# Optimization experiments

Hardware: AMD Instinct MI355X
Metric: run time of the kernel (lower is better)

Reference implementation:

```python
import jax, jax.numpy as jnp
import numpy as np

N = 12288      # nodes
E = 393216     # edges (avg degree 32)
D_IN = 512
D_H = 256      # interm_dim
D_Z = 64       # latent_dim


def setup_inputs() -> dict:
    key = jax.random.key(0)
    ks = jax.random.split(key, 9)
    X = jax.random.normal(ks[0], (N, D_IN), jnp.float32)
    edge_index = jax.random.randint(ks[1], (2, E), 0, N, dtype=jnp.int64)
    # GCNConv weights (glorot-ish scaling)
    W1 = jax.random.normal(ks[2], (D_IN, D_H), jnp.float32) / np.sqrt(D_IN)
    b1 = jnp.zeros((D_H,), jnp.float32)
    Wmu = jax.random.normal(ks[3], (D_H, D_Z), jnp.float32) / np.sqrt(D_H)
    bmu = jnp.zeros((D_Z,), jnp.float32)
    Wsig = jax.random.normal(ks[4], (D_H, 1), jnp.float32) / np.sqrt(D_H)
    bsig = jnp.zeros((1,), jnp.float32)
    # reparameterization noise (torch: Normal(0,1).sample(mus.size()))
    eps = jax.random.normal(ks[5], (N, D_Z), jnp.float32)
    return {"X": X, "edge_index": edge_index, "W1": W1, "b1": b1,
            "Wmu": Wmu, "bmu": bmu, "Wsig": Wsig, "bsig": bsig, "eps": eps}


def _gcn_conv(h_in, W, b, src, dst, norm):
    # GCNConv: linear transform then symmetric-normalized aggregation with self-loops
    h = h_in @ W + b                                   # [N, F_out]
    msg = h[src] * norm[src, None]                     # gather + scale
    agg = jax.ops.segment_sum(msg, dst, num_segments=N)
    # self-loop contribution: norm_i * norm_i * h_i
    return norm[:, None] * (agg + norm[:, None] * h)


def reference(X, edge_index, W1, b1, Wmu, bmu, Wsig, bsig, eps):
    src, dst = edge_index[0], edge_index[1]
    # degree of A + I (edge weight 1, plus self loop)
    deg = jax.ops.segment_sum(jnp.ones((E,), X.dtype), dst, num_segments=N) + 1.0
    norm = jax.lax.rsqrt(deg)                          # D^{-1/2}

    # encoder
    H = jax.nn.relu(_gcn_conv(X, W1, b1, src, dst, norm))   # [N, D_H]; dropout p=0.0
    mus = _gcn_conv(H, Wmu, bmu, src, dst, norm)            # [N, D_Z]
    logsigma2s = _gcn_conv(H, Wsig, bsig, src, dst, norm)   # [N, 1]

    # reparameterize
    sigmas = jnp.exp(0.5 * logsigma2s)                      # [N, 1]
    Z = mus + sigmas * eps                                  # [N, D_Z]

    # dense decoder
    ZZt = Z @ Z.T                                           # [N, N]
    return ZZt, mus, logsigma2s
```

## Files before the change

kernel.cpp:

```cpp
#include <hip/hip_runtime.h>

#define N_NODES 12288
#define N_EDGES 393216
#define DIN 512
#define DH 256
#define DZ 64

typedef __bf16 bf16x8 __attribute__((ext_vector_type(8)));
typedef float f32x4 __attribute__((ext_vector_type(4)));
typedef unsigned short u16x8 __attribute__((ext_vector_type(8)));

static __device__ __forceinline__ unsigned short f2bf(float f) {
    unsigned int u = __float_as_uint(f);
    unsigned int r = (u + 0x7fffu + ((u >> 16) & 1u)) >> 16;
    return (unsigned short)r;
}
static __device__ __forceinline__ float bf2f(unsigned short u) {
    return __uint_as_float((unsigned int)u << 16);
}

__global__ __launch_bounds__(256) void k_prep(const float* __restrict__ X, unsigned short* __restrict__ Xb,
                                              const float* __restrict__ W1, unsigned short* __restrict__ W1T,
                                              const float* __restrict__ Wmu, unsigned short* __restrict__ WmuT,
                                              const int* __restrict__ dst, int* __restrict__ deg) {
    int b = blockIdx.x;
    if (b < 6144) {
        int i = b * 256 + threadIdx.x;
        float4 v = ((const float4*)X)[i];
        ushort4 o;
        o.x = f2bf(v.x); o.y = f2bf(v.y); o.z = f2bf(v.z); o.w = f2bf(v.w);
        ((ushort4*)Xb)[i] = o;
    } else if (b < 6656) {
        int i = (b - 6144) * 256 + threadIdx.x;
        int c = i >> 9, k = i & 511;
        W1T[i] = f2bf(W1[k * DH + c]);
    } else if (b < 6720) {
        int i = (b - 6656) * 256 + threadIdx.x;
        int c = i >> 8, k = i & 255;
        WmuT[i] = f2bf(Wmu[k * DZ + c]);
    } else {
        int e = (b - 6720) * 256 + threadIdx.x;
        atomicAdd(&deg[dst[e]], 1);
    }
}

__global__ __launch_bounds__(512) void k_sg(const unsigned short* __restrict__ Xb,
                                            const unsigned short* __restrict__ W1T,
                                            const float* __restrict__ b1, const int* __restrict__ deg,
                                            float* __restrict__ norm, unsigned short* __restrict__ g1,
                                            const int* __restrict__ src, const int* __restrict__ dst,
                                            int* __restrict__ rp, int* __restrict__ cursor,
                                            int* __restrict__ ssrc, int* __restrict__ flag) {
    __shared__ int sp[512];
    if (blockIdx.x < 96) {
        int j = blockIdx.x;
        int wid = threadIdx.x >> 6;
        int lane = threadIdx.x & 63;
        int ln = lane & 15, kg = lane >> 4;
        int rb = (j >> 1) * 256 + (wid >> 1) * 64;
        int cb = (j & 1) * 128 + (wid & 1) * 64;
        f32x4 acc[4][4] = {};
        const unsigned short* xa = Xb + (size_t)(rb + ln) * DIN + kg * 8;
        const unsigned short* wb = W1T + (size_t)(cb + ln) * DIN + kg * 8;
        for (int ks = 0; ks < 16; ++ks) {
            int k0 = ks * 32;
            bf16x8 a[4], b[4];
#pragma unroll
            for (int m = 0; m < 4; ++m) a[m] = *(const bf16x8*)(xa + (size_t)m * 16 * DIN + k0);
#pragma unroll
            for (int n = 0; n < 4; ++n) b[n] = *(const bf16x8*)(wb + (size_t)n * 16 * DIN + k0);
#pragma unroll
            for (int m = 0; m < 4; ++m)
#pragma unroll
                for (int n = 0; n < 4; ++n)
                    acc[m][n] = __builtin_amdgcn_mfma_f32_16x16x32_bf16(a[m], b[n], acc[m][n], 0, 0, 0);
        }
#pragma unroll
        for (int m = 0; m < 4; ++m)
#pragma unroll
            for (int r = 0; r < 4; ++r) {
                int row = rb + m * 16 + kg * 4 + r;
                float ni = rsqrtf((float)deg[row] + 1.0f);
#pragma unroll
                for (int n = 0; n < 4; ++n) {
                    int col = cb + n * 16 + ln;
                    g1[(size_t)row * DH + col] = f2bf(ni * (acc[m][n][r] + b1[col]));
                }
            }
    } else {
        int t = threadIdx.x;
        if (blockIdx.x == 96) {
            int base = t * 24;
            int loc[24];
            int s = 0;
#pragma unroll
            for (int j = 0; j < 24; ++j) {
                int c = deg[base + j];
                norm[base + j] = rsqrtf((float)c + 1.0f);
                cursor[base + j] = 0;
                loc[j] = s; s += c;
            }
            sp[t] = s;
            __syncthreads();
            for (int off = 1; off < 512; off <<= 1) {
                int v = (t >= off) ? sp[t - off] : 0;
                __syncthreads();
                sp[t] += v;
                __syncthreads();
            }
            int pre = (t == 0) ? 0 : sp[t - 1];
#pragma unroll
            for (int j = 0; j < 24; ++j) rp[base + j] = pre + loc[j];
            if (t == 511) rp[N_NODES] = sp[511];
            __threadfence();
            __syncthreads();
            if (t == 0)
                __hip_atomic_store(flag, 1, __ATOMIC_RELEASE, __HIP_MEMORY_SCOPE_AGENT);
        } else {
            if (t == 0) {
                while (__hip_atomic_load(flag, __ATOMIC_RELAXED, __HIP_MEMORY_SCOPE_AGENT) == 0)
                    __builtin_amdgcn_s_sleep(8);
                (void)__hip_atomic_load(flag, __ATOMIC_ACQUIRE, __HIP_MEMORY_SCOPE_AGENT);
            }
            __syncthreads();
        }
        int base = (blockIdx.x - 96) * 512 + t;
#pragma unroll
        for (int e = base; e < N_EDGES; e += 192 * 512) {
            int d = dst[e];
            int pos = atomicAdd(&cursor[d], 1);
            ssrc[rp[d] + pos] = src[e];
        }
    }
}

__global__ __launch_bounds__(256) void k_agg1(const unsigned short* __restrict__ g1,
                                              const int* __restrict__ rp, const int* __restrict__ ssrc,
                                              const float* __restrict__ norm, const float* __restrict__ Wsig,
                                              unsigned short* __restrict__ G2, float* __restrict__ tvec,
                                              float* __restrict__ qv) {
    int w = threadIdx.x >> 6;
    int lane = threadIdx.x & 63;
    int half = lane >> 5, lh = lane & 31;
    int i = blockIdx.x * 4 + w;
    int beg = rp[i], end = rp[i + 1];
    int itn = (end - beg + 1) >> 1;
    size_t cho = (size_t)lh * 8;
    float a8[8] = {};
    float ssum = 0.f;
#pragma unroll 2
    for (int it = 0; it < itn; ++it) {
        int e = beg + it * 2 + half;
        if (e < end) {
            int s = ssrc[e];
            u16x8 v = *(const u16x8*)(g1 + ((size_t)s << 8) + cho);
            ssum += norm[s];
#pragma unroll
            for (int j = 0; j < 8; ++j) a8[j] += bf2f(v[j]);
        }
    }
    if (half == 0) {
        u16x8 v = *(const u16x8*)(g1 + ((size_t)i << 8) + cho);
#pragma unroll
        for (int j = 0; j < 8; ++j) a8[j] += bf2f(v[j]);
    }
#pragma unroll
    for (int j = 0; j < 8; ++j) a8[j] += __shfl_xor(a8[j], 32);
    ssum += __shfl_xor(ssum, 32);
    float ni = norm[i];
    const float4 ws0 = *(const float4*)(Wsig + cho);
    const float4 ws1 = *(const float4*)(Wsig + cho + 4);
    float g[8];
#pragma unroll
    for (int j = 0; j < 8; ++j) g[j] = ni * fmaxf(ni * a8[j], 0.f);
    float qp = g[0] * ws0.x + g[1] * ws0.y + g[2] * ws0.z + g[3] * ws0.w
             + g[4] * ws1.x + g[5] * ws1.y + g[6] * ws1.z + g[7] * ws1.w;
    if (half == 0) {
        u16x8 o;
#pragma unroll
        for (int j = 0; j < 8; ++j) o[j] = f2bf(g[j]);
        *(u16x8*)(G2 + ((size_t)i << 8) + cho) = o;
    }
#pragma unroll
    for (int m = 16; m >= 1; m >>= 1) qp += __shfl_xor(qp, m);
    if (lane == 0) {
        tvec[i] = ssum + ni;
        qv[i] = qp;
    }
}

__global__ __launch_bounds__(256) void k_gemm2(const unsigned short* __restrict__ G2,
                                               const unsigned short* __restrict__ WmuT,
                                               unsigned short* __restrict__ Pb) {
    int wid = threadIdx.x >> 6;
    int lane = threadIdx.x & 63;
    int ln = lane & 15, kg = lane >> 4;
    int rb = blockIdx.x * 128 + wid * 32;
    f32x4 acc[2][4] = {};
    const unsigned short* xa = G2 + (size_t)(rb + ln) * DH + kg * 8;
    const unsigned short* wb = WmuT + (size_t)ln * DH + kg * 8;
    for (int ks = 0; ks < 8; ++ks) {
        int k0 = ks * 32;
        bf16x8 a[2], b[4];
#pragma unroll
        for (int m = 0; m < 2; ++m) a[m] = *(const bf16x8*)(xa + (size_t)m * 16 * DH + k0);
#pragma unroll
        for (int n = 0; n < 4; ++n) b[n] = *(const bf16x8*)(wb + (size_t)n * 16 * DH + k0);
#pragma unroll
        for (int m = 0; m < 2; ++m)
#pragma unroll
            for (int n = 0; n < 4; ++n)
                acc[m][n] = __builtin_amdgcn_mfma_f32_16x16x32_bf16(a[m], b[n], acc[m][n], 0, 0, 0);
    }
#pragma unroll
    for (int m = 0; m < 2; ++m)
#pragma unroll
        for (int n = 0; n < 4; ++n)
#pragma unroll
            for (int r = 0; r < 4; ++r) {
                int row = rb + m * 16 + kg * 4 + r;
                int col = n * 16 + ln;
                Pb[(size_t)row * DZ + col] = f2bf(acc[m][n][r]);
            }
}

__global__ __launch_bounds__(256) void k_agg2(const unsigned short* __restrict__ Pb,
                                              const float* __restrict__ qv,
                                              const int* __restrict__ rp, const int* __restrict__ ssrc,
                                              const float* __restrict__ norm, const float* __restrict__ tvec,
                                              const float* __restrict__ bmu, const float* __restrict__ bsig,
                                              const float* __restrict__ eps,
                                              float* __restrict__ mus_out, float* __restrict__ logs_out,
                                              unsigned short* __restrict__ Zb) {
    int w = threadIdx.x >> 6;
    int lane = threadIdx.x & 63;
    int grp = lane >> 4, li = lane & 15;
    int i = blockIdx.x * 4 + w;
    int beg = rp[i], end = rp[i + 1];
    int itn = (end - beg + 3) >> 2;
    int co = li * 4;
    float a4[4] = {};
    float qa = 0.f;
#pragma unroll 2
    for (int it = 0; it < itn; ++it) {
        int e = beg + it * 4 + grp;
        if (e < end) {
            int s = ssrc[e];
            ushort4 v = *(const ushort4*)(Pb + ((size_t)s << 6) + co);
            qa += qv[s];
            a4[0] += bf2f(v.x); a4[1] += bf2f(v.y); a4[2] += bf2f(v.z); a4[3] += bf2f(v.w);
        }
    }
    if (grp == 0) {
        ushort4 v = *(const ushort4*)(Pb + ((size_t)i << 6) + co);
        qa += qv[i];
        a4[0] += bf2f(v.x); a4[1] += bf2f(v.y); a4[2] += bf2f(v.z); a4[3] += bf2f(v.w);
    }
#pragma unroll
    for (int j = 0; j < 4; ++j) {
        a4[j] += __shfl_xor(a4[j], 16);
        a4[j] += __shfl_xor(a4[j], 32);
    }
    qa += __shfl_xor(qa, 16);
    qa += __shfl_xor(qa, 32);
    float ni = norm[i], tv = tvec[i];
    float ls = ni * (qa + bsig[0] * tv);
    float sig = expf(0.5f * ls);
    if (lane == 0) logs_out[i] = ls;
    if (lane < 16) {
        const float4 bm = *(const float4*)(bmu + co);
        float4 mu;
        mu.x = ni * (a4[0] + bm.x * tv);
        mu.y = ni * (a4[1] + bm.y * tv);
        mu.z = ni * (a4[2] + bm.z * tv);
        mu.w = ni * (a4[3] + bm.w * tv);
        size_t oidx = ((size_t)i << 6) + co;
        *(float4*)(mus_out + oidx) = mu;
        const float4 ep = *(const float4*)(eps + oidx);
        ushort4 z;
        z.x = f2bf(mu.x + sig * ep.x);
        z.y = f2bf(mu.y + sig * ep.y);
        z.z = f2bf(mu.z + sig * ep.z);
        z.w = f2bf(mu.w + sig * ep.w);
        *(ushort4*)(Zb + oidx) = z;
    }
}

#define LPAD 260
__global__ __launch_bounds__(256) void k_zzt(const unsigned short* __restrict__ Zb, float* __restrict__ out) {
    __shared__ float lds[32 * LPAD];
    int w = threadIdx.x >> 6;
    int lane = threadIdx.x & 63;
    int ln = lane & 15, kg = lane >> 4;
    int rb = blockIdx.x * 64;
    int cb = blockIdx.y * 256 + w * 64;
    bf16x8 a[4][2], b[4][2];
#pragma unroll
    for (int m = 0; m < 4; ++m)
#pragma unroll
        for (int kc = 0; kc < 2; ++kc)
            a[m][kc] = *(const bf16x8*)(Zb + (size_t)(rb + m * 16 + ln) * DZ + kc * 32 + kg * 8);
#pragma unroll
    for (int n = 0; n < 4; ++n)
#pragma unroll
        for (int kc = 0; kc < 2; ++kc)
            b[n][kc] = *(const bf16x8*)(Zb + (size_t)(cb + n * 16 + ln) * DZ + kc * 32 + kg * 8);
    f32x4 acc[4][4] = {};
#pragma unroll
    for (int m = 0; m < 4; ++m)
#pragma unroll
        for (int n = 0; n < 4; ++n) {
            acc[m][n] = __builtin_amdgcn_mfma_f32_16x16x32_bf16(a[m][0], b[n][0], acc[m][n], 0, 0, 0);
            acc[m][n] = __builtin_amdgcn_mfma_f32_16x16x32_bf16(a[m][1], b[n][1], acc[m][n], 0, 0, 0);
        }
    int c4 = (threadIdx.x & 63) * 4;
    int rw = threadIdx.x >> 6;
    size_t colbase = (size_t)blockIdx.y * 256 + c4;
#pragma unroll
    for (int p = 0; p < 2; ++p) {
        if (p) __syncthreads();
#pragma unroll
        for (int mm = 0; mm < 2; ++mm) {
            int m = p * 2 + mm;
#pragma unroll
            for (int n = 0; n < 4; ++n)
#pragma unroll
                for (int r = 0; r < 4; ++r)
                    lds[(mm * 16 + kg * 4 + r) * LPAD + w * 64 + n * 16 + ln] = acc[m][n][r];
        }
        __syncthreads();
#pragma unroll
        for (int it = 0; it < 8; ++it) {
            int rl = it * 4 + rw;
            f32x4 v = *(const f32x4*)&lds[rl * LPAD + c4];
            __builtin_nontemporal_store(v, (f32x4*)(out + (size_t)(rb + p * 32 + rl) * N_NODES + colbase));
        }
    }
}

extern "C" void kernel_launch(void* const* d_in, const int* in_sizes, int n_in,
                              void* d_out, int out_size, void* d_ws, size_t ws_size,
                              hipStream_t stream) {
    const float* X = (const float*)d_in[0];
    const int* edge = (const int*)d_in[1];
    const float* W1 = (const float*)d_in[2];
    const float* b1 = (const float*)d_in[3];
    const float* Wmu = (const float*)d_in[4];
    const float* bmu = (const float*)d_in[5];
    const float* Wsig = (const float*)d_in[6];
    const float* bsig = (const float*)d_in[7];
    const float* eps = (const float*)d_in[8];

    const int* esrc = edge;
    const int* edst = edge + N_EDGES;

    char* w = (char*)d_ws;
    int* flag = (int*)w;           w += 64;
    int* deg = (int*)w;            w += (size_t)N_NODES * 4;
    int* cursor = (int*)w;         w += (size_t)N_NODES * 4;
    float* norm = (float*)w;       w += (size_t)N_NODES * 4;
    float* tvec = (float*)w;       w += (size_t)N_NODES * 4;
    float* qv = (float*)w;         w += (size_t)N_NODES * 4;
    int* rowptr = (int*)w;         w += (size_t)(N_NODES + 64) * 4;
    int* ssrc = (int*)w;           w += (size_t)N_EDGES * 4;
    unsigned short* Xb = (unsigned short*)w;   w += (size_t)N_NODES * DIN * 2;
    unsigned short* W1T = (unsigned short*)w;  w += (size_t)DIN * DH * 2;
    unsigned short* WmuT = (unsigned short*)w; w += (size_t)DH * DZ * 2;
    unsigned short* g1 = (unsigned short*)w;   w += (size_t)N_NODES * DH * 2;
    unsigned short* G2 = (unsigned short*)w;   w += (size_t)N_NODES * DH * 2;
    unsigned short* Pb = (unsigned short*)w;   w += (size_t)N_NODES * DZ * 2;
    unsigned short* Zb = (unsigned short*)w;   w += (size_t)N_NODES * DZ * 2;

    float* out_zzt = (float*)d_out;
    float* out_mus = out_zzt + (size_t)N_NODES * N_NODES;
    float* out_logs = out_mus + (size_t)N_NODES * DZ;

    (void)hipMemsetAsync(d_ws, 0, 64 + (size_t)N_NODES * 4, stream);
    k_prep<<<8256, 256, 0, stream>>>(X, Xb, W1, W1T, Wmu, WmuT, edst, deg);
    k_sg<<<288, 512, 0, stream>>>(Xb, W1T, b1, deg, norm, g1, esrc, edst, rowptr, cursor, ssrc, flag);
    k_agg1<<<N_NODES / 4, 256, 0, stream>>>(g1, rowptr, ssrc, norm, Wsig, G2, tvec, qv);
    k_gemm2<<<N_NODES / 128, 256, 0, stream>>>(G2, WmuT, Pb);
    k_agg2<<<N_NODES / 4, 256, 0, stream>>>(Pb, qv, rowptr, ssrc, norm, tvec, bmu, bsig, eps,
                                            out_mus, out_logs, Zb);
    k_zzt<<<dim3(N_NODES / 64, N_NODES / 256), 256, 0, stream>>>(Zb, out_zzt);
}
```

Baseline: 260.3 us.

## Fuse agg1, gemm2 and agg2 into one persistent kernel with grid barriers

Merges the first aggregation, the small mu GEMM and the second aggregation into a single persistent kernel of 2048 blocks. Software grid-wide barriers built on agent-scope atomics replace the kernel boundaries. Nodes are processed in a grid-stride loop, and the GEMM is split into 16-row tiles per wave. This removes two kernel launches and their inter-kernel gaps. It relies on all 2048 blocks being co-resident, otherwise the spin barrier deadlocks, and it adds barrier spin cost.

```diff
diff --git a/kernel.cpp b/kernel.cpp
--- a/kernel.cpp
+++ b/kernel.cpp
@@ -5,6 +5,7 @@
 #define DIN 512
 #define DH 256
 #define DZ 64
+#define NBA 2048
 
 typedef __bf16 bf16x8 __attribute__((ext_vector_type(8)));
 typedef float f32x4 __attribute__((ext_vector_type(4)));
@@ -17,6 +18,17 @@
 }
 static __device__ __forceinline__ float bf2f(unsigned short u) {
     return __uint_as_float((unsigned int)u << 16);
+}
+
+static __device__ __forceinline__ void gridbar(int* bar, int p, int nb) {
+    __syncthreads();
+    if (threadIdx.x == 0) {
+        __hip_atomic_fetch_add(&bar[p], 1, __ATOMIC_RELEASE, __HIP_MEMORY_SCOPE_AGENT);
+        while (__hip_atomic_load(&bar[p], __ATOMIC_RELAXED, __HIP_MEMORY_SCOPE_AGENT) < nb)
+            __builtin_amdgcn_s_sleep(8);
+        (void)__hip_atomic_load(&bar[p], __ATOMIC_ACQUIRE, __HIP_MEMORY_SCOPE_AGENT);
+    }
+    __syncthreads();
 }
 
 __global__ __launch_bounds__(256) void k_prep(const float* __restrict__ X, unsigned short* __restrict__ Xb,
@@ -134,155 +146,150 @@
     }
 }
 
-__global__ __launch_bounds__(256) void k_agg1(const unsigned short* __restrict__ g1,
-                                              const int* __restrict__ rp, const int* __restrict__ ssrc,
-                                              const float* __restrict__ norm, const float* __restrict__ Wsig,
-                                              unsigned short* __restrict__ G2, float* __restrict__ tvec,
-                                              float* __restrict__ qv) {
+__global__ __launch_bounds__(256, 8) void k_a12(
+    const unsigned short* __restrict__ g1,
+    const int* __restrict__ rp, const int* __restrict__ ssrc,
+    const float* __restrict__ norm, const float* __restrict__ Wsig,
+    const unsigned short* __restrict__ WmuT,
+    unsigned short* __restrict__ G2, float* __restrict__ tvec, float* __restrict__ qv,
+    unsigned short* __restrict__ Pb,
+    const float* __restrict__ bmu, const float* __restrict__ bsig,
+    const float* __restrict__ eps,
+    float* __restrict__ mus_out, float* __restrict__ logs_out,
+    unsigned short* __restrict__ Zb, int* __restrict__ bar) {
+
     int w = threadIdx.x >> 6;
     int lane = threadIdx.x & 63;
-    int half = lane >> 5, lh = lane & 31;
-    int i = blockIdx.x * 4 + w;
-    int beg = rp[i], end = rp[i + 1];
-    int itn = (end - beg + 1) >> 1;
-    size_t cho = (size_t)lh * 8;
-    float a8[8] = {};
-    float ssum = 0.f;
+    int gw = blockIdx.x * 4 + w;
+
+    {
+        int half = lane >> 5, lh = lane & 31;
+        size_t cho = (size_t)lh * 8;
+        for (int i = gw; i < N_NODES; i += 8192) {
+            int beg = rp[i], end = rp[i + 1];
+            int itn = (end - beg + 1) >> 1;
+            float a8[8] = {};
+            float ssum = 0.f;
 #pragma unroll 2
-    for (int it = 0; it < itn; ++it) {
-        int e = beg + it * 2 + half;
-        if (e < end) {
-            int s = ssrc[e];
-            u16x8 v = *(const u16x8*)(g1 + ((size_t)s << 8) + cho);
-            ssum += norm[s];
-#pragma unroll
-            for (int j = 0; j < 8; ++j) a8[j] += bf2f(v[j]);
-        }
-    }
-    if (half == 0) {
-        u16x8 v = *(const u16x8*)(g1 + ((size_t)i << 8) + cho);
-#pragma unroll
-        for (int j = 0; j < 8; ++j) a8[j] += bf2f(v[j]);
-    }
-#pragma unroll
-    for (int j = 0; j < 8; ++j) a8[j] += __shfl_xor(a8[j], 32);
-    ssum += __shfl_xor(ssum, 32);
-    float ni = norm[i];
-    const float4 ws0 = *(const float4*)(Wsig + cho);
-    const float4 ws1 = *(const float4*)(Wsig + cho + 4);
-    float g[8];
-#pragma unroll
-    for (int j = 0; j < 8; ++j) g[j] = ni * fmaxf(ni * a8[j], 0.f);
-    float qp = g[0] * ws0.x + g[1] * ws0.y + g[2] * ws0.z + g[3] * ws0.w
-             + g[4] * ws1.x + g[5] * ws1.y + g[6] * ws1.z + g[7] * ws1.w;
-    if (half == 0) {
-        u16x8 o;
-#pragma unroll
-        for (int j = 0; j < 8; ++j) o[j] = f2bf(g[j]);
-        *(u16x8*)(G2 + ((size_t)i << 8) + cho) = o;
-    }
-#pragma unroll
-    for (int m = 16; m >= 1; m >>= 1) qp += __shfl_xor(qp, m);
-    if (lane == 0) {
-        tvec[i] = ssum + ni;
-        qv[i] = qp;
-    }
-}
-
-__global__ __launch_bounds__(256) void k_gemm2(const unsigned short* __restrict__ G2,
-                                               const unsigned short* __restrict__ WmuT,
-                                               unsigned short* __restrict__ Pb) {
-    int wid = threadIdx.x >> 6;
-    int lane = threadIdx.x & 63;
-    int ln = lane & 15, kg = lane >> 4;
-    int rb = blockIdx.x * 128 + wid * 32;
-    f32x4 acc[2][4] = {};
-    const unsigned short* xa = G2 + (size_t)(rb + ln) * DH + kg * 8;
-    const unsigned short* wb = WmuT + (size_t)ln * DH + kg * 8;
-    for (int ks = 0; ks < 8; ++ks) {
-        int k0 = ks * 32;
-        bf16x8 a[2], b[4];
-#pragma unroll
-        for (int m = 0; m < 2; ++m) a[m] = *(const bf16x8*)(xa + (size_t)m * 16 * DH + k0);
-#pragma unroll
-        for (int n = 0; n < 4; ++n) b[n] = *(const bf16x8*)(wb + (size_t)n * 16 * DH + k0);
-#pragma unroll
-        for (int m = 0; m < 2; ++m)
+            for (int it = 0; it < itn; ++it) {
+                int e = beg + it * 2 + half;
+                if (e < end) {
+                    int s = ssrc[e];
+                    u16x8 v = *(const u16x8*)(g1 + ((size_t)s << 8) + cho);
+                    ssum += norm[s];
+#pragma unroll
+                    for (int j = 0; j < 8; ++j) a8[j] += bf2f(v[j]);
+                }
+            }
+            if (half == 0) {
+                u16x8 v = *(const u16x8*)(g1 + ((size_t)i << 8) + cho);
+#pragma unroll
+                for (int j = 0; j < 8; ++j) a8[j] += bf2f(v[j]);
+            }
+#pragma unroll
+            for (int j = 0; j < 8; ++j) a8[j] += __shfl_xor(a8[j], 32);
+            ssum += __shfl_xor(ssum, 32);
+            float ni = norm[i];
+            const float4 ws0 = *(const float4*)(Wsig + cho);
+            const float4 ws1 = *(const float4*)(Wsig + cho + 4);
+            float g[8];
+#pragma unroll
+            for (int j = 0; j < 8; ++j) g[j] = ni * fmaxf(ni * a8[j], 0.f);
+            float qp = g[0] * ws0.x + g[1] * ws0.y + g[2] * ws0.z + g[3] * ws0.w
+                     + g[4] * ws1.x + g[5] * ws1.y + g[6] * ws1.z + g[7] * ws1.w;
+            if (half == 0) {
+                u16x8 o;
+#pragma unroll
+                for (int j = 0; j < 8; ++j) o[j] = f2bf(g[j]);
+                *(u16x8*)(G2 + ((size_t)i << 8) + cho) = o;
+            }
+#pragma unroll
+            for (int m = 16; m >= 1; m >>= 1) qp += __shfl_xor(qp, m);
+            if (lane == 0) {
+                tvec[i] = ssum + ni;
+                qv[i] = qp;
+            }
+        }
+    }
+    gridbar(bar, 0, NBA);
+
+    if (gw < 768) {
+        int ln = lane & 15, kg = lane >> 4;
+        int rb = gw * 16;
+        f32x4 acc[4] = {};
+        const unsigned short* xa = G2 + (size_t)(rb + ln) * DH + kg * 8;
+        const unsigned short* wb = WmuT + (size_t)ln * DH + kg * 8;
+#pragma unroll
+        for (int ks = 0; ks < 8; ++ks) {
+            int k0 = ks * 32;
+            bf16x8 a = *(const bf16x8*)(xa + k0);
+            bf16x8 b[4];
+#pragma unroll
+            for (int n = 0; n < 4; ++n) b[n] = *(const bf16x8*)(wb + (size_t)n * 16 * DH + k0);
 #pragma unroll
             for (int n = 0; n < 4; ++n)
-                acc[m][n] = __builtin_amdgcn_mfma_f32_16x16x32_bf16(a[m], b[n], acc[m][n], 0, 0, 0);
-    }
-#pragma unroll
-    for (int m = 0; m < 2; ++m)
+                acc[n] = __builtin_amdgcn_mfma_f32_16x16x32_bf16(a, b[n], acc[n], 0, 0, 0);
+        }
 #pragma unroll
         for (int n = 0; n < 4; ++n)
 #pragma unroll
-            for (int r = 0; r < 4; ++r) {
-                int row = rb + m * 16 + kg * 4 + r;
-                int col = n * 16 + ln;
-                Pb[(size_t)row * DZ + col] = f2bf(acc[m][n][r]);
-            }
-}
-
-__global__ __launch_bounds__(256) void k_agg2(const unsigned short* __restrict__ Pb,
-                                              const float* __restrict__ qv,
-                                              const int* __restrict__ rp, const int* __restrict__ ssrc,
-                                              const float* __restrict__ norm, const float* __restrict__ tvec,
-                                              const float* __restrict__ bmu, const float* __restrict__ bsig,
-                                              const float* __restrict__ eps,
-                                              float* __restrict__ mus_out, float* __restrict__ logs_out,
-                                              unsigned short* __restrict__ Zb) {
-    int w = threadIdx.x >> 6;
-    int lane = threadIdx.x & 63;
-    int grp = lane >> 4, li = lane & 15;
-    int i = blockIdx.x * 4 + w;
-    int beg = rp[i], end = rp[i + 1];
-    int itn = (end - beg + 3) >> 2;
-    int co = li * 4;
-    float a4[4] = {};
-    float qa = 0.f;
+            for (int r = 0; r < 4; ++r)
+                Pb[(size_t)(rb + kg * 4 + r) * DZ + n * 16 + ln] = f2bf(acc[n][r]);
+    }
+    gridbar(bar, 1, NBA);
+
+    {
+        int grp = lane >> 4, li = lane & 15;
+        int co = li * 4;
+        for (int i = gw; i < N_NODES; i += 8192) {
+            int beg = rp[i], end = rp[i + 1];
+            int itn = (end - beg + 3) >> 2;
+            float a4[4] = {};
+            float qa = 0.f;
 #pragma unroll 2
-    for (int it = 0; it < itn; ++it) {
-        int e = beg + it * 4 + grp;
-        if (e < end) {
-            int s = ssrc[e];
-            ushort4 v = *(const ushort4*)(Pb + ((size_t)s << 6) + co);
-            qa += qv[s];
-            a4[0] += bf2f(v.x); a4[1] += bf2f(v.y); a4[2] += bf2f(v.z); a4[3] += bf2f(v.w);
-        }
-    }
-    if (grp == 0) {
-        ushort4 v = *(const ushort4*)(Pb + ((size_t)i << 6) + co);
-        qa += qv[i];
-        a4[0] += bf2f(v.x); a4[1] += bf2f(v.y); a4[2] += bf2f(v.z); a4[3] += bf2f(v.w);
-    }
-#pragma unroll
-    for (int j = 0; j < 4; ++j) {
-        a4[j] += __shfl_xor(a4[j], 16);
-        a4[j] += __shfl_xor(a4[j], 32);
-    }
-    qa += __shfl_xor(qa, 16);
-    qa += __shfl_xor(qa, 32);
-    float ni = norm[i], tv = tvec[i];
-    float ls = ni * (qa + bsig[0] * tv);
-    float sig = expf(0.5f * ls);
-    if (lane == 0) logs_out[i] = ls;
-    if (lane < 16) {
-        const float4 bm = *(const float4*)(bmu + co);
-        float4 mu;
-        mu.x = ni * (a4[0] + bm.x * tv);
-        mu.y = ni * (a4[1] + bm.y * tv);
-        mu.z = ni * (a4[2] + bm.z * tv);
-        mu.w = ni * (a4[3] + bm.w * tv);
-        size_t oidx = ((size_t)i << 6) + co;
-        *(float4*)(mus_out + oidx) = mu;
-        const float4 ep = *(const float4*)(eps + oidx);
-        ushort4 z;
-        z.x = f2bf(mu.x + sig * ep.x);
-        z.y = f2bf(mu.y + sig * ep.y);
-        z.z = f2bf(mu.z + sig * ep.z);
-        z.w = f2bf(mu.w + sig * ep.w);
-        *(ushort4*)(Zb + oidx) = z;
+            for (int it = 0; it < itn; ++it) {
+                int e = beg + it * 4 + grp;
+                if (e < end) {
+                    int s = ssrc[e];
+                    ushort4 v = *(const ushort4*)(Pb + ((size_t)s << 6) + co);
+                    qa += qv[s];
+                    a4[0] += bf2f(v.x); a4[1] += bf2f(v.y); a4[2] += bf2f(v.z); a4[3] += bf2f(v.w);
+                }
+            }
+            if (grp == 0) {
+                ushort4 v = *(const ushort4*)(Pb + ((size_t)i << 6) + co);
+                qa += qv[i];
+                a4[0] += bf2f(v.x); a4[1] += bf2f(v.y); a4[2] += bf2f(v.z); a4[3] += bf2f(v.w);
+            }
+#pragma unroll
+            for (int j = 0; j < 4; ++j) {
+                a4[j] += __shfl_xor(a4[j], 16);
+                a4[j] += __shfl_xor(a4[j], 32);
+            }
+            qa += __shfl_xor(qa, 16);
+            qa += __shfl_xor(qa, 32);
+            float ni = norm[i], tv = tvec[i];
+            float ls = ni * (qa + bsig[0] * tv);
+            float sig = expf(0.5f * ls);
+            if (lane == 0) logs_out[i] = ls;
+            if (lane < 16) {
+                const float4 bm = *(const float4*)(bmu + co);
+                float4 mu;
+                mu.x = ni * (a4[0] + bm.x * tv);
+                mu.y = ni * (a4[1] + bm.y * tv);
+                mu.z = ni * (a4[2] + bm.z * tv);
+                mu.w = ni * (a4[3] + bm.w * tv);
+                size_t oidx = ((size_t)i << 6) + co;
+                *(float4*)(mus_out + oidx) = mu;
+                const float4 ep = *(const float4*)(eps + oidx);
+                ushort4 z;
+                z.x = f2bf(mu.x + sig * ep.x);
+                z.y = f2bf(mu.y + sig * ep.y);
+                z.z = f2bf(mu.z + sig * ep.z);
+                z.w = f2bf(mu.w + sig * ep.w);
+                *(ushort4*)(Zb + oidx) = z;
+            }
+        }
     }
 }
 
@@ -355,7 +362,8 @@
     const int* edst = edge + N_EDGES;
 
     char* w = (char*)d_ws;
-    int* flag = (int*)w;           w += 64;
+    int* flag = (int*)w;
+    int* bar = (int*)w + 1;        w += 64;
     int* deg = (int*)w;            w += (size_t)N_NODES * 4;
     int* cursor = (int*)w;         w += (size_t)N_NODES * 4;
     float* norm = (float*)w;       w += (size_t)N_NODES * 4;
@@ -378,9 +386,7 @@
     (void)hipMemsetAsync(d_ws, 0, 64 + (size_t)N_NODES * 4, stream);
     k_prep<<<8256, 256, 0, stream>>>(X, Xb, W1, W1T, Wmu, WmuT, edst, deg);
     k_sg<<<288, 512, 0, stream>>>(Xb, W1T, b1, deg, norm, g1, esrc, edst, rowptr, cursor, ssrc, flag);
-    k_agg1<<<N_NODES / 4, 256, 0, stream>>>(g1, rowptr, ssrc, norm, Wsig, G2, tvec, qv);
-    k_gemm2<<<N_NODES / 128, 256, 0, stream>>>(G2, WmuT, Pb);
-    k_agg2<<<N_NODES / 4, 256, 0, stream>>>(Pb, qv, rowptr, ssrc, norm, tvec, bmu, bsig, eps,
-                                            out_mus, out_logs, Zb);
+    k_a12<<<NBA, 256, 0, stream>>>(g1, rowptr, ssrc, norm, Wsig, WmuT, G2, tvec, qv, Pb,
+                                   bmu, bsig, eps, out_mus, out_logs, Zb, bar);
     k_zzt<<<dim3(N_NODES / 64, N_NODES / 256), 256, 0, stream>>>(Zb, out_zzt);
 }
```

New measurement: 679.7 us. +161.1%, slower.
